# Optimization experiments

Measured on AMD Instinct MI355X. Metric: run time of the kernel, lower is better.

Reference implementation:

```python
import jax, jax.numpy as jnp
import numpy as np

B, C, H, W = 4, 512, 64, 64
CQ = C // 8


def setup_inputs() -> dict:
    key = jax.random.key(0)
    k1, k2, k3, k4, k5 = jax.random.split(key, 5)
    return {
        "x": jax.random.normal(k1, (B, C, H, W), dtype=jnp.float32),
        "Wq": jax.random.normal(k2, (CQ, C), dtype=jnp.float32) * (2.0 / C) ** 0.5,
        "Wk": jax.random.normal(k3, (CQ, C), dtype=jnp.float32) * (2.0 / C) ** 0.5,
        "Wv": jax.random.normal(k4, (C, C), dtype=jnp.float32) * (2.0 / C) ** 0.5,
        "gamma": jax.random.normal(k5, (1,), dtype=jnp.float32),
    }


def reference(x, Wq, Wk, Wv, gamma):
    b, c, h, w = x.shape
    n = h * w
    xf = x.reshape(b, c, n)                       # (B, C, N)
    # 1x1 convs (bias=False, norm=identity) == channel matmuls
    q = jnp.einsum('qc,bcn->bnq', Wq, xf)         # (B, N, Cq) -- proj_query permuted
    k = jnp.einsum('qc,bcm->bqm', Wk, xf)         # (B, Cq, N) -- proj_key
    energy = jnp.einsum('bnq,bqm->bnm', q, k)     # (B, N, N)
    attn = jax.nn.softmax(energy, axis=-1)        # softmax over keys (last dim)
    v = jnp.einsum('dc,bcm->bdm', Wv, xf)         # (B, C, N) -- proj_value
    # out = bmm(V, attn^T): out[b,d,n] = sum_m V[b,d,m] * attn[b,n,m]
    out = jnp.einsum('bdm,bnm->bdn', v, attn).reshape(b, c, h, w)
    return gamma * out + x
```

## Files before the change

kernel.cpp:

```cpp
#include <hip/hip_runtime.h>

#define B_  4
#define C_  512
#define CQ_ 64
#define N_  4096
#define LOG2E 1.44269504088896f

typedef _Float16 half8 __attribute__((ext_vector_type(8)));
typedef _Float16 half4 __attribute__((ext_vector_type(4)));
typedef float    f32x4 __attribute__((ext_vector_type(4)));

__device__ __forceinline__ void g2l16(const void* g, void* l) {
  __builtin_amdgcn_global_load_lds(
      (const __attribute__((address_space(1))) void*)g,
      (__attribute__((address_space(3))) void*)l, 16, 0, 0);
}

__global__ __launch_bounds__(256) void wcvt_kernel(
    const float* __restrict__ Wq, const float* __restrict__ Wk,
    const float* __restrict__ Wv, _Float16* __restrict__ Wh)
{
  const int row = blockIdx.x;
  const float* src;
  float s = 1.0f;
  if (row < 64)       { src = Wq + (size_t)row * C_; s = LOG2E; }
  else if (row < 128) { src = Wk + (size_t)(row - 64) * C_; }
  else                { src = Wv + (size_t)(row - 128) * C_; }
  for (int c = threadIdx.x; c < C_; c += 256)
    Wh[(size_t)row * C_ + c] = (_Float16)(src[c] * s);
}

__global__ __launch_bounds__(256) void proj_kernel(
    const float* __restrict__ x, const _Float16* __restrict__ Wh,
    _Float16* __restrict__ Qh, _Float16* __restrict__ Kh, _Float16* __restrict__ Vh)
{
  __shared__ _Float16 xs[32][520];
  __shared__ _Float16 vs[64][40];

  const int tid = threadIdx.x;
  const int wid = tid >> 6, lane = tid & 63, ln = lane & 15, lh = lane >> 4;

  const int wg = (blockIdx.x & 7) * 64 + (blockIdx.x >> 3);
  const int b  = wg >> 7;
  const int n0 = (wg & 127) * 32;

  {
    const int nn = (tid & 7) * 4;
    const int c0 = tid >> 3;
    #pragma unroll 4
    for (int cc = 0; cc < 16; ++cc) {
      const int c = cc * 32 + c0;
      f32x4 v = *(const f32x4*)&x[((size_t)b * C_ + c) * N_ + n0 + nn];
      #pragma unroll
      for (int u = 0; u < 4; ++u) xs[nn + u][c] = (_Float16)v[u];
    }
  }
  __syncthreads();

  for (int chT = 0; chT < 10; ++chT) {
    f32x4 acc[2] = {};
    const _Float16* wrow = Wh + (size_t)(chT * 64 + wid * 16 + ln) * C_;

    #pragma unroll 4
    for (int kt = 0; kt < C_; kt += 32) {
      half8 a = *(const half8*)&wrow[kt + lh * 8];
      #pragma unroll
      for (int ct = 0; ct < 2; ++ct) {
        half8 bf = *(const half8*)&xs[ct * 16 + ln][kt + lh * 8];
        acc[ct] = __builtin_amdgcn_mfma_f32_16x16x32_f16(a, bf, acc[ct], 0, 0, 0);
      }
    }

    if (chT < 2) {
      #pragma unroll
      for (int ct = 0; ct < 2; ++ct) {
        const int n = n0 + ct * 16 + ln;
        #pragma unroll
        for (int j = 0; j < 4; ++j) {
          const int chL = wid * 16 + lh * 4 + j;
          const _Float16 v = (_Float16)acc[ct][j];
          if (chT == 0) Qh[((size_t)b * N_ + n) * CQ_ + chL] = v;
          else          Kh[((size_t)b * N_ + n) * CQ_ + chL] = v;
        }
      }
    } else {
      __syncthreads();
      #pragma unroll
      for (int ct = 0; ct < 2; ++ct)
        #pragma unroll
        for (int j = 0; j < 4; ++j)
          vs[wid * 16 + lh * 4 + j][ct * 16 + ln] = (_Float16)acc[ct][j];
      __syncthreads();
      const int row = tid >> 2, cb = (tid & 3) * 8;
      *(half8*)&Vh[((size_t)b * C_ + (chT - 2) * 64 + row) * N_ + n0 + cb] =
          *(const half8*)&vs[row][cb];
    }
  }
}

__global__ __launch_bounds__(512, 2) void stats_kernel(
    const _Float16* __restrict__ Qh, const _Float16* __restrict__ Kh,
    float* __restrict__ m_g, float* __restrict__ il_g)
{
  __shared__ float Ms[8][64];
  __shared__ float Ss[8][64];

  const int tid = threadIdx.x;
  const int wid = tid >> 6, lane = tid & 63, ln = lane & 15, lh = lane >> 4;
  const int b  = blockIdx.x >> 6;
  const int qb = (blockIdx.x & 63) * 64;

  half8 qf[4][2];
  #pragma unroll
  for (int rt = 0; rt < 4; ++rt)
    #pragma unroll
    for (int h = 0; h < 2; ++h)
      qf[rt][h] = *(const half8*)&Qh[((size_t)b * N_ + qb + rt * 16 + ln) * CQ_ + h * 32 + lh * 8];

  float mx[4] = {-3.0e38f, -3.0e38f, -3.0e38f, -3.0e38f};
  float sm[4] = {0.f, 0.f, 0.f, 0.f};

  const _Float16* kp = Kh + ((size_t)b * N_ + wid * 16 + ln) * CQ_ + lh * 8;

  half8 k0 = *(const half8*)kp;
  half8 k1 = *(const half8*)(kp + 32);

  for (int it = 0; it < 32; ++it) {
    half8 kn0, kn1;
    if (it < 31) {
      const _Float16* kq = kp + (size_t)((it + 1) * 128) * CQ_;
      kn0 = *(const half8*)kq;
      kn1 = *(const half8*)(kq + 32);
    }
    #pragma unroll
    for (int rt = 0; rt < 4; ++rt) {
      f32x4 e = {};
      e = __builtin_amdgcn_mfma_f32_16x16x32_f16(k0, qf[rt][0], e, 0, 0, 0);
      e = __builtin_amdgcn_mfma_f32_16x16x32_f16(k1, qf[rt][1], e, 0, 0, 0);
      const float m1 = fmaxf(fmaxf(e[0], e[1]), fmaxf(e[2], e[3]));
      const float mn = fmaxf(mx[rt], m1);
      sm[rt] = sm[rt] * exp2f(mx[rt] - mn)
             + exp2f(e[0] - mn) + exp2f(e[1] - mn)
             + exp2f(e[2] - mn) + exp2f(e[3] - mn);
      mx[rt] = mn;
    }
    k0 = kn0; k1 = kn1;
  }

  #pragma unroll
  for (int rt = 0; rt < 4; ++rt) {
    float m = mx[rt], s = sm[rt];
    #pragma unroll
    for (int mask = 16; mask <= 32; mask <<= 1) {
      const float om = __shfl_xor(m, mask);
      const float os = __shfl_xor(s, mask);
      const float mn = fmaxf(m, om);
      s = s * exp2f(m - mn) + os * exp2f(om - mn);
      m = mn;
    }
    if (lane < 16) { Ms[wid][rt * 16 + lane] = m; Ss[wid][rt * 16 + lane] = s; }
  }
  __syncthreads();
  if (tid < 64) {
    float m = Ms[0][tid], s = Ss[0][tid];
    #pragma unroll
    for (int w = 1; w < 8; ++w) {
      const float om = Ms[w][tid], os = Ss[w][tid];
      const float mn = fmaxf(m, om);
      s = s * exp2f(m - mn) + os * exp2f(om - mn);
      m = mn;
    }
    m_g[(size_t)b * N_ + qb + tid]  = m;
    il_g[(size_t)b * N_ + qb + tid] = 1.0f / s;
  }
}

__global__ __launch_bounds__(256) void pwrite_kernel(
    const _Float16* __restrict__ Qh, const _Float16* __restrict__ Kh,
    const float* __restrict__ m_g, const float* __restrict__ il_g,
    _Float16* __restrict__ P, int b0)
{
  __shared__ _Float16 Pl[64 * 260];

  const int tid = threadIdx.x;
  const int wid = tid >> 6, lane = tid & 63, ln = lane & 15, lh = lane >> 4;
  const int mb = blockIdx.x * 256;
  const int qb = blockIdx.y * 64;
  const int bz = blockIdx.z;
  const int b  = b0 + bz;

  float m_l[4], il_l[4];
  #pragma unroll
  for (int rt = 0; rt < 4; ++rt) {
    m_l[rt]  = m_g [(size_t)b * N_ + qb + rt * 16 + ln];
    il_l[rt] = il_g[(size_t)b * N_ + qb + rt * 16 + ln];
  }

  half8 qf[4][2];
  #pragma unroll
  for (int rt = 0; rt < 4; ++rt)
    #pragma unroll
    for (int h = 0; h < 2; ++h)
      qf[rt][h] = *(const half8*)&Qh[((size_t)b * N_ + qb + rt * 16 + ln) * CQ_ + h * 32 + lh * 8];

  half8 kf[4][2];
  #pragma unroll
  for (int ms = 0; ms < 4; ++ms)
    #pragma unroll
    for (int h = 0; h < 2; ++h)
      kf[ms][h] = *(const half8*)&Kh[((size_t)b * N_ + mb + wid * 64 + ms * 16 + ln) * CQ_ + h * 32 + lh * 8];

  #pragma unroll
  for (int ms = 0; ms < 4; ++ms) {
    #pragma unroll
    for (int rt = 0; rt < 4; ++rt) {
      f32x4 e = {};
      e = __builtin_amdgcn_mfma_f32_16x16x32_f16(kf[ms][0], qf[rt][0], e, 0, 0, 0);
      e = __builtin_amdgcn_mfma_f32_16x16x32_f16(kf[ms][1], qf[rt][1], e, 0, 0, 0);
      half4 pv;
      #pragma unroll
      for (int j = 0; j < 4; ++j)
        pv[j] = (_Float16)(exp2f(e[j] - m_l[rt]) * il_l[rt]);
      *(half4*)&Pl[(rt * 16 + ln) * 260 + wid * 64 + ms * 16 + lh * 4] = pv;
    }
  }
  __syncthreads();

  const int row = tid >> 2;
  const int cb  = (tid & 3) * 8;
  #pragma unroll
  for (int i = 0; i < 8; ++i) {
    half8 v = *(const half8*)&Pl[row * 260 + cb + i * 32];
    *(half8*)&P[((size_t)bz * N_ + qb + row) * N_ + mb + cb + i * 32] = v;
  }
}

__global__ __launch_bounds__(512) void pv_kernel(
    const float* __restrict__ x, const _Float16* __restrict__ Vh,
    const _Float16* __restrict__ P, const float* __restrict__ gamma,
    float* __restrict__ out, int b0, int nwg)
{
  __shared__ _Float16 As[3][256 * 64];
  __shared__ _Float16 Bs[3][128 * 64];

  const int tid = threadIdx.x;
  const int wid = tid >> 6, lane = tid & 63, ln = lane & 15, lh = lane >> 4;

  const int q8 = nwg >> 3;
  const int wg = (blockIdx.x & 7) * q8 + (blockIdx.x >> 3);
  const int dt = wg & 1;
  const int nt = (wg >> 1) & 31;
  const int bz = wg >> 6;
  const int b  = b0 + bz;
  const int d0 = dt * 256, n0 = nt * 128;

  const _Float16* Ab = Vh + ((size_t)b * C_ + d0) * N_;
  const _Float16* Bb = P  + ((size_t)bz * N_ + n0) * N_;

  const int srow   = lane >> 3;
  const int schunk = lane & 7;
  const _Float16* aSrc[4];
  const _Float16* bSrc[2];
  #pragma unroll
  for (int r = 0; r < 4; ++r) {
    const int row = r * 64 + wid * 8 + srow;
    aSrc[r] = Ab + (size_t)row * N_ + ((schunk ^ (row & 7)) << 3);
  }
  #pragma unroll
  for (int r = 0; r < 2; ++r) {
    const int row = r * 64 + wid * 8 + srow;
    bSrc[r] = Bb + (size_t)row * N_ + ((schunk ^ (row & 7)) << 3);
  }

  auto stage = [&](int buf, int t) {
    const int m0 = t << 6;
    #pragma unroll
    for (int r = 0; r < 4; ++r)
      g2l16(aSrc[r] + m0, (char*)&As[buf][0] + r * 8192 + wid * 1024);
    #pragma unroll
    for (int r = 0; r < 2; ++r)
      g2l16(bSrc[r] + m0, (char*)&Bs[buf][0] + r * 8192 + wid * 1024);
  };

  const int wr = wid >> 1, wc = wid & 1;
  f32x4 acc[4][4] = {};
  const int swl = ln & 7;

  stage(0, 0);
  stage(1, 1);

  for (int t = 0; t < 64; ++t) {
    if (t < 63) { asm volatile("s_waitcnt vmcnt(6)" ::: "memory"); }
    else        { asm volatile("s_waitcnt vmcnt(0)" ::: "memory"); }
    __builtin_amdgcn_s_barrier();
    __builtin_amdgcn_sched_barrier(0);

    const int buf = t % 3;
    const _Float16* Ar = &As[buf][0];
    const _Float16* Br = &Bs[buf][0];

    half8 a[4][2], bq[4][2];
    #pragma unroll
    for (int ft = 0; ft < 4; ++ft) {
      const int row = wr * 64 + ft * 16 + ln;
      #pragma unroll
      for (int kk = 0; kk < 2; ++kk)
        a[ft][kk] = *(const half8*)&Ar[row * 64 + ((((kk << 2) | lh) ^ swl) << 3)];
    }
    #pragma unroll
    for (int gt = 0; gt < 4; ++gt) {
      const int row = wc * 64 + gt * 16 + ln;
      #pragma unroll
      for (int kk = 0; kk < 2; ++kk)
        bq[gt][kk] = *(const half8*)&Br[row * 64 + ((((kk << 2) | lh) ^ swl) << 3)];
    }

    if (t < 62) stage((t + 2) % 3, t + 2);

    #pragma unroll
    for (int kk = 0; kk < 2; ++kk)
      #pragma unroll
      for (int ft = 0; ft < 4; ++ft)
        #pragma unroll
        for (int gt = 0; gt < 4; ++gt)
          acc[ft][gt] = __builtin_amdgcn_mfma_f32_16x16x32_f16(a[ft][kk], bq[gt][kk], acc[ft][gt], 0, 0, 0);
  }

  const float g = gamma[0];
  #pragma unroll
  for (int ft = 0; ft < 4; ++ft) {
    #pragma unroll
    for (int gt = 0; gt < 4; ++gt) {
      #pragma unroll
      for (int j = 0; j < 4; ++j) {
        const int d = d0 + wr * 64 + ft * 16 + lh * 4 + j;
        const int n = n0 + wc * 64 + gt * 16 + ln;
        const size_t idx = ((size_t)b * C_ + d) * N_ + n;
        out[idx] = g * acc[ft][gt][j] + x[idx];
      }
    }
  }
}

extern "C" void kernel_launch(void* const* d_in, const int* in_sizes, int n_in,
                              void* d_out, int out_size, void* d_ws, size_t ws_size,
                              hipStream_t stream) {
  const float* x     = (const float*)d_in[0];
  const float* Wq    = (const float*)d_in[1];
  const float* Wk    = (const float*)d_in[2];
  const float* Wv    = (const float*)d_in[3];
  const float* gamma = (const float*)d_in[4];
  float* out = (float*)d_out;

  _Float16* Qh = (_Float16*)d_ws;
  _Float16* Kh = Qh + (size_t)B_ * N_ * CQ_;
  _Float16* Vh = Kh + (size_t)B_ * N_ * CQ_;
  float* m_g   = (float*)(Vh + (size_t)B_ * C_ * N_);
  float* il_g  = m_g + (size_t)B_ * N_;
  _Float16* Wh = (_Float16*)(il_g + (size_t)B_ * N_);
  _Float16* P  = Wh + (size_t)640 * C_;

  const size_t fixed = (size_t)((char*)P - (char*)d_ws);
  const int nb = (ws_size >= fixed + (size_t)B_ * N_ * N_ * sizeof(_Float16)) ? 4 : 2;

  wcvt_kernel<<<dim3(640), 256, 0, stream>>>(Wq, Wk, Wv, Wh);
  proj_kernel<<<dim3(512), 256, 0, stream>>>(x, Wh, Qh, Kh, Vh);
  stats_kernel<<<dim3(256), 512, 0, stream>>>(Qh, Kh, m_g, il_g);

  for (int b0 = 0; b0 < B_; b0 += nb) {
    pwrite_kernel<<<dim3(16, 64, nb), 256, 0, stream>>>(Qh, Kh, m_g, il_g, P, b0);
    pv_kernel<<<dim3(nb * 64), 512, 0, stream>>>(x, Vh, P, gamma, out, b0, nb * 64);
  }
}
```

Baseline: 185.6 us.

## Fuse probability computation into PV kernel, eliminating materialized attention matrix

Replaces the separate pwrite and pv kernels with one fused kernel. Each workgroup recomputes QK^T scores per key tile from staged K, applies the precomputed max and inverse sum to form P in LDS, and then multiplies by V. This removes the write and reread of the full fp16 N×N attention matrix in global memory. In exchange, each workgroup recomputes scores (the two d-tiles duplicate that work), adds an extra barrier per iteration, and serialises exp work with the MFMA pipeline.

```diff
diff --git a/kernel.cpp b/kernel.cpp
--- a/kernel.cpp
+++ b/kernel.cpp
@@ -175,166 +175,138 @@
   }
 }
 
-__global__ __launch_bounds__(256) void pwrite_kernel(
-    const _Float16* __restrict__ Qh, const _Float16* __restrict__ Kh,
+__global__ __launch_bounds__(512) void fpv_kernel(
+    const float* __restrict__ x, const _Float16* __restrict__ Qh,
+    const _Float16* __restrict__ Kh, const _Float16* __restrict__ Vh,
     const float* __restrict__ m_g, const float* __restrict__ il_g,
-    _Float16* __restrict__ P, int b0)
+    const float* __restrict__ gamma, float* __restrict__ out)
 {
-  __shared__ _Float16 Pl[64 * 260];
+  __shared__ _Float16 As[3][256 * 64];
+  __shared__ _Float16 Ks[3][64 * 64];
+  __shared__ _Float16 Ps[128 * 64];
 
   const int tid = threadIdx.x;
   const int wid = tid >> 6, lane = tid & 63, ln = lane & 15, lh = lane >> 4;
-  const int mb = blockIdx.x * 256;
-  const int qb = blockIdx.y * 64;
-  const int bz = blockIdx.z;
-  const int b  = b0 + bz;
-
-  float m_l[4], il_l[4];
-  #pragma unroll
-  for (int rt = 0; rt < 4; ++rt) {
-    m_l[rt]  = m_g [(size_t)b * N_ + qb + rt * 16 + ln];
-    il_l[rt] = il_g[(size_t)b * N_ + qb + rt * 16 + ln];
-  }
-
-  half8 qf[4][2];
-  #pragma unroll
-  for (int rt = 0; rt < 4; ++rt)
-    #pragma unroll
-    for (int h = 0; h < 2; ++h)
-      qf[rt][h] = *(const half8*)&Qh[((size_t)b * N_ + qb + rt * 16 + ln) * CQ_ + h * 32 + lh * 8];
-
-  half8 kf[4][2];
-  #pragma unroll
-  for (int ms = 0; ms < 4; ++ms)
-    #pragma unroll
-    for (int h = 0; h < 2; ++h)
-      kf[ms][h] = *(const half8*)&Kh[((size_t)b * N_ + mb + wid * 64 + ms * 16 + ln) * CQ_ + h * 32 + lh * 8];
-
-  #pragma unroll
-  for (int ms = 0; ms < 4; ++ms) {
-    #pragma unroll
-    for (int rt = 0; rt < 4; ++rt) {
-      f32x4 e = {};
-      e = __builtin_amdgcn_mfma_f32_16x16x32_f16(kf[ms][0], qf[rt][0], e, 0, 0, 0);
-      e = __builtin_amdgcn_mfma_f32_16x16x32_f16(kf[ms][1], qf[rt][1], e, 0, 0, 0);
-      half4 pv;
-      #pragma unroll
-      for (int j = 0; j < 4; ++j)
-        pv[j] = (_Float16)(exp2f(e[j] - m_l[rt]) * il_l[rt]);
-      *(half4*)&Pl[(rt * 16 + ln) * 260 + wid * 64 + ms * 16 + lh * 4] = pv;
-    }
-  }
-  __syncthreads();
-
-  const int row = tid >> 2;
-  const int cb  = (tid & 3) * 8;
-  #pragma unroll
-  for (int i = 0; i < 8; ++i) {
-    half8 v = *(const half8*)&Pl[row * 260 + cb + i * 32];
-    *(half8*)&P[((size_t)bz * N_ + qb + row) * N_ + mb + cb + i * 32] = v;
-  }
-}
-
-__global__ __launch_bounds__(512) void pv_kernel(
-    const float* __restrict__ x, const _Float16* __restrict__ Vh,
-    const _Float16* __restrict__ P, const float* __restrict__ gamma,
-    float* __restrict__ out, int b0, int nwg)
-{
-  __shared__ _Float16 As[3][256 * 64];
-  __shared__ _Float16 Bs[3][128 * 64];
-
-  const int tid = threadIdx.x;
-  const int wid = tid >> 6, lane = tid & 63, ln = lane & 15, lh = lane >> 4;
-
-  const int q8 = nwg >> 3;
-  const int wg = (blockIdx.x & 7) * q8 + (blockIdx.x >> 3);
+
+  const int wg = (blockIdx.x & 7) * 32 + (blockIdx.x >> 3);
   const int dt = wg & 1;
   const int nt = (wg >> 1) & 31;
-  const int bz = wg >> 6;
-  const int b  = b0 + bz;
+  const int b  = wg >> 6;
   const int d0 = dt * 256, n0 = nt * 128;
 
-  const _Float16* Ab = Vh + ((size_t)b * C_ + d0) * N_;
-  const _Float16* Bb = P  + ((size_t)bz * N_ + n0) * N_;
+  const float m2  = m_g [(size_t)b * N_ + n0 + wid * 16 + ln];
+  const float il2 = il_g[(size_t)b * N_ + n0 + wid * 16 + ln];
+
+  half8 qf[2];
+  #pragma unroll
+  for (int h = 0; h < 2; ++h)
+    qf[h] = *(const half8*)&Qh[((size_t)b * N_ + n0 + wid * 16 + ln) * CQ_ + h * 32 + lh * 8];
 
   const int srow   = lane >> 3;
   const int schunk = lane & 7;
   const _Float16* aSrc[4];
-  const _Float16* bSrc[2];
   #pragma unroll
   for (int r = 0; r < 4; ++r) {
     const int row = r * 64 + wid * 8 + srow;
-    aSrc[r] = Ab + (size_t)row * N_ + ((schunk ^ (row & 7)) << 3);
-  }
-  #pragma unroll
-  for (int r = 0; r < 2; ++r) {
-    const int row = r * 64 + wid * 8 + srow;
-    bSrc[r] = Bb + (size_t)row * N_ + ((schunk ^ (row & 7)) << 3);
+    aSrc[r] = Vh + ((size_t)b * C_ + d0 + row) * N_ + ((schunk ^ (row & 7)) << 3);
+  }
+  const _Float16* kSrc;
+  {
+    const int row = wid * 8 + srow;
+    kSrc = Kh + ((size_t)b * N_ + row) * CQ_ + ((schunk ^ (row & 7)) << 3);
   }
 
   auto stage = [&](int buf, int t) {
-    const int m0 = t << 6;
+    const int mA = t << 6;
     #pragma unroll
     for (int r = 0; r < 4; ++r)
-      g2l16(aSrc[r] + m0, (char*)&As[buf][0] + r * 8192 + wid * 1024);
-    #pragma unroll
-    for (int r = 0; r < 2; ++r)
-      g2l16(bSrc[r] + m0, (char*)&Bs[buf][0] + r * 8192 + wid * 1024);
+      g2l16(aSrc[r] + mA, (char*)&As[buf][0] + r * 8192 + wid * 1024);
+    g2l16(kSrc + (size_t)(t << 6) * CQ_, (char*)&Ks[buf][0] + wid * 1024);
   };
 
-  const int wr = wid >> 1, wc = wid & 1;
+  const int dr = wid >> 1, nc = wid & 1;
+  const int swl = ln & 7;
   f32x4 acc[4][4] = {};
-  const int swl = ln & 7;
 
   stage(0, 0);
   stage(1, 1);
 
   for (int t = 0; t < 64; ++t) {
-    if (t < 63) { asm volatile("s_waitcnt vmcnt(6)" ::: "memory"); }
+    if (t < 63) { asm volatile("s_waitcnt vmcnt(5)" ::: "memory"); }
     else        { asm volatile("s_waitcnt vmcnt(0)" ::: "memory"); }
     __builtin_amdgcn_s_barrier();
     __builtin_amdgcn_sched_barrier(0);
 
     const int buf = t % 3;
-    const _Float16* Ar = &As[buf][0];
-    const _Float16* Br = &Bs[buf][0];
-
-    half8 a[4][2], bq[4][2];
-    #pragma unroll
-    for (int ft = 0; ft < 4; ++ft) {
-      const int row = wr * 64 + ft * 16 + ln;
-      #pragma unroll
-      for (int kk = 0; kk < 2; ++kk)
-        a[ft][kk] = *(const half8*)&Ar[row * 64 + ((((kk << 2) | lh) ^ swl) << 3)];
-    }
+
+    {
+      const _Float16* Kr = &Ks[buf][0];
+      half8 kf[4][2];
+      #pragma unroll
+      for (int kt = 0; kt < 4; ++kt) {
+        const int key = kt * 16 + ln;
+        #pragma unroll
+        for (int c = 0; c < 2; ++c)
+          kf[kt][c] = *(const half8*)&Kr[key * 64 + ((((c << 2) | lh) ^ swl) << 3)];
+      }
+
+      if (t < 62) stage((t + 2) % 3, t + 2);
+
+      #pragma unroll
+      for (int kt = 0; kt < 4; ++kt) {
+        f32x4 e = {};
+        e = __builtin_amdgcn_mfma_f32_16x16x32_f16(kf[kt][0], qf[0], e, 0, 0, 0);
+        e = __builtin_amdgcn_mfma_f32_16x16x32_f16(kf[kt][1], qf[1], e, 0, 0, 0);
+        half4 pv;
+        #pragma unroll
+        for (int j = 0; j < 4; ++j)
+          pv[j] = (_Float16)(exp2f(e[j] - m2) * il2);
+        *(half4*)((char*)&Ps[(wid * 16 + ln) * 64]
+                  + ((((kt << 1) | (lh >> 1)) ^ swl) << 4) + ((lh & 1) << 3)) = pv;
+      }
+    }
+
+    asm volatile("s_waitcnt lgkmcnt(0)" ::: "memory");
+    __builtin_amdgcn_sched_barrier(0);
+    __builtin_amdgcn_s_barrier();
+    __builtin_amdgcn_sched_barrier(0);
+
+    {
+      const _Float16* Ar = &As[buf][0];
+      half8 a[4][2], bq[4][2];
+      #pragma unroll
+      for (int ft = 0; ft < 4; ++ft) {
+        const int row = dr * 64 + ft * 16 + ln;
+        #pragma unroll
+        for (int c = 0; c < 2; ++c)
+          a[ft][c] = *(const half8*)&Ar[row * 64 + ((((c << 2) | lh) ^ swl) << 3)];
+      }
+      #pragma unroll
+      for (int gt = 0; gt < 4; ++gt) {
+        const int q = nc * 64 + gt * 16 + ln;
+        #pragma unroll
+        for (int c = 0; c < 2; ++c)
+          bq[gt][c] = *(const half8*)&Ps[q * 64 + ((((c << 2) | lh) ^ swl) << 3)];
+      }
+      #pragma unroll
+      for (int c = 0; c < 2; ++c)
+        #pragma unroll
+        for (int ft = 0; ft < 4; ++ft)
+          #pragma unroll
+          for (int gt = 0; gt < 4; ++gt)
+            acc[ft][gt] = __builtin_amdgcn_mfma_f32_16x16x32_f16(a[ft][c], bq[gt][c], acc[ft][gt], 0, 0, 0);
+    }
+  }
+
+  const float g = gamma[0];
+  #pragma unroll
+  for (int ft = 0; ft < 4; ++ft) {
     #pragma unroll
     for (int gt = 0; gt < 4; ++gt) {
-      const int row = wc * 64 + gt * 16 + ln;
-      #pragma unroll
-      for (int kk = 0; kk < 2; ++kk)
-        bq[gt][kk] = *(const half8*)&Br[row * 64 + ((((kk << 2) | lh) ^ swl) << 3)];
-    }
-
-    if (t < 62) stage((t + 2) % 3, t + 2);
-
-    #pragma unroll
-    for (int kk = 0; kk < 2; ++kk)
-      #pragma unroll
-      for (int ft = 0; ft < 4; ++ft)
-        #pragma unroll
-        for (int gt = 0; gt < 4; ++gt)
-          acc[ft][gt] = __builtin_amdgcn_mfma_f32_16x16x32_f16(a[ft][kk], bq[gt][kk], acc[ft][gt], 0, 0, 0);
-  }
-
-  const float g = gamma[0];
-  #pragma unroll
-  for (int ft = 0; ft < 4; ++ft) {
-    #pragma unroll
-    for (int gt = 0; gt < 4; ++gt) {
       #pragma unroll
       for (int j = 0; j < 4; ++j) {
-        const int d = d0 + wr * 64 + ft * 16 + lh * 4 + j;
-        const int n = n0 + wc * 64 + gt * 16 + ln;
+        const int d = d0 + dr * 64 + ft * 16 + lh * 4 + j;
+        const int n = n0 + nc * 64 + gt * 16 + ln;
         const size_t idx = ((size_t)b * C_ + d) * N_ + n;
         out[idx] = g * acc[ft][gt][j] + x[idx];
       }
@@ -358,17 +330,9 @@
   float* m_g   = (float*)(Vh + (size_t)B_ * C_ * N_);
   float* il_g  = m_g + (size_t)B_ * N_;
   _Float16* Wh = (_Float16*)(il_g + (size_t)B_ * N_);
-  _Float16* P  = Wh + (size_t)640 * C_;
-
-  const size_t fixed = (size_t)((char*)P - (char*)d_ws);
-  const int nb = (ws_size >= fixed + (size_t)B_ * N_ * N_ * sizeof(_Float16)) ? 4 : 2;
 
   wcvt_kernel<<<dim3(640), 256, 0, stream>>>(Wq, Wk, Wv, Wh);
   proj_kernel<<<dim3(512), 256, 0, stream>>>(x, Wh, Qh, Kh, Vh);
   stats_kernel<<<dim3(256), 512, 0, stream>>>(Qh, Kh, m_g, il_g);
-
-  for (int b0 = 0; b0 < B_; b0 += nb) {
-    pwrite_kernel<<<dim3(16, 64, nb), 256, 0, stream>>>(Qh, Kh, m_g, il_g, P, b0);
-    pv_kernel<<<dim3(nb * 64), 512, 0, stream>>>(x, Vh, P, gamma, out, b0, nb * 64);
-  }
-}
+  fpv_kernel<<<dim3(256), 512, 0, stream>>>(x, Qh, Kh, Vh, m_g, il_g, gamma, out);
+}
```

Result: slower. 195.2 us (+5.2%).

## Split PV GEMM K-step into two half phases with interleaved staging and setprio

Applied to the files above, without the earlier changes.

Splits each 64-wide K tile of the output GEMM into two 32-wide halves. Each half reads its own LDS fragments, issues half of the next-next tile's global-to-LDS loads, and runs its MFMAs under raised wave priority, with an extra barrier between the halves. The aim is to interleave load issue with MFMA work, lower register pressure from fragment buffers, and let waves in the MFMA phase keep priority. The risk is the extra barrier per iteration. The vmcnt(6) wait still matches six outstanding loads per stage, now issued in two groups of three.

```diff
diff --git a/kernel.cpp b/kernel.cpp
--- a/kernel.cpp
+++ b/kernel.cpp
@@ -272,22 +272,25 @@
     bSrc[r] = Bb + (size_t)row * N_ + ((schunk ^ (row & 7)) << 3);
   }
 
-  auto stage = [&](int buf, int t) {
+  auto stageA = [&](int buf, int t) {
     const int m0 = t << 6;
-    #pragma unroll
-    for (int r = 0; r < 4; ++r)
-      g2l16(aSrc[r] + m0, (char*)&As[buf][0] + r * 8192 + wid * 1024);
-    #pragma unroll
-    for (int r = 0; r < 2; ++r)
-      g2l16(bSrc[r] + m0, (char*)&Bs[buf][0] + r * 8192 + wid * 1024);
+    g2l16(aSrc[0] + m0, (char*)&As[buf][0] + 0 * 8192 + wid * 1024);
+    g2l16(aSrc[1] + m0, (char*)&As[buf][0] + 1 * 8192 + wid * 1024);
+    g2l16(bSrc[0] + m0, (char*)&Bs[buf][0] + 0 * 8192 + wid * 1024);
+  };
+  auto stageB = [&](int buf, int t) {
+    const int m0 = t << 6;
+    g2l16(aSrc[2] + m0, (char*)&As[buf][0] + 2 * 8192 + wid * 1024);
+    g2l16(aSrc[3] + m0, (char*)&As[buf][0] + 3 * 8192 + wid * 1024);
+    g2l16(bSrc[1] + m0, (char*)&Bs[buf][0] + 1 * 8192 + wid * 1024);
   };
 
   const int wr = wid >> 1, wc = wid & 1;
   f32x4 acc[4][4] = {};
   const int swl = ln & 7;
 
-  stage(0, 0);
-  stage(1, 1);
+  stageA(0, 0); stageB(0, 0);
+  stageA(1, 1); stageB(1, 1);
 
   for (int t = 0; t < 64; ++t) {
     if (t < 63) { asm volatile("s_waitcnt vmcnt(6)" ::: "memory"); }
@@ -299,31 +302,53 @@
     const _Float16* Ar = &As[buf][0];
     const _Float16* Br = &Bs[buf][0];
 
-    half8 a[4][2], bq[4][2];
-    #pragma unroll
-    for (int ft = 0; ft < 4; ++ft) {
-      const int row = wr * 64 + ft * 16 + ln;
-      #pragma unroll
-      for (int kk = 0; kk < 2; ++kk)
-        a[ft][kk] = *(const half8*)&Ar[row * 64 + ((((kk << 2) | lh) ^ swl) << 3)];
-    }
-    #pragma unroll
-    for (int gt = 0; gt < 4; ++gt) {
-      const int row = wc * 64 + gt * 16 + ln;
-      #pragma unroll
-      for (int kk = 0; kk < 2; ++kk)
-        bq[gt][kk] = *(const half8*)&Br[row * 64 + ((((kk << 2) | lh) ^ swl) << 3)];
-    }
-
-    if (t < 62) stage((t + 2) % 3, t + 2);
-
-    #pragma unroll
-    for (int kk = 0; kk < 2; ++kk)
+    {
+      half8 a[4], bq[4];
+      #pragma unroll
+      for (int ft = 0; ft < 4; ++ft) {
+        const int row = wr * 64 + ft * 16 + ln;
+        a[ft] = *(const half8*)&Ar[row * 64 + ((lh ^ swl) << 3)];
+      }
+      #pragma unroll
+      for (int gt = 0; gt < 4; ++gt) {
+        const int row = wc * 64 + gt * 16 + ln;
+        bq[gt] = *(const half8*)&Br[row * 64 + ((lh ^ swl) << 3)];
+      }
+      if (t < 62) stageA((t + 2) % 3, t + 2);
+
+      __builtin_amdgcn_s_setprio(1);
       #pragma unroll
       for (int ft = 0; ft < 4; ++ft)
         #pragma unroll
         for (int gt = 0; gt < 4; ++gt)
-          acc[ft][gt] = __builtin_amdgcn_mfma_f32_16x16x32_f16(a[ft][kk], bq[gt][kk], acc[ft][gt], 0, 0, 0);
+          acc[ft][gt] = __builtin_amdgcn_mfma_f32_16x16x32_f16(a[ft], bq[gt], acc[ft][gt], 0, 0, 0);
+      __builtin_amdgcn_s_setprio(0);
+    }
+    __builtin_amdgcn_s_barrier();
+    __builtin_amdgcn_sched_barrier(0);
+
+    {
+      half8 a[4], bq[4];
+      #pragma unroll
+      for (int ft = 0; ft < 4; ++ft) {
+        const int row = wr * 64 + ft * 16 + ln;
+        a[ft] = *(const half8*)&Ar[row * 64 + (((4 | lh) ^ swl) << 3)];
+      }
+      #pragma unroll
+      for (int gt = 0; gt < 4; ++gt) {
+        const int row = wc * 64 + gt * 16 + ln;
+        bq[gt] = *(const half8*)&Br[row * 64 + (((4 | lh) ^ swl) << 3)];
+      }
+      if (t < 62) stageB((t + 2) % 3, t + 2);
+
+      __builtin_amdgcn_s_setprio(1);
+      #pragma unroll
+      for (int ft = 0; ft < 4; ++ft)
+        #pragma unroll
+        for (int gt = 0; gt < 4; ++gt)
+          acc[ft][gt] = __builtin_amdgcn_mfma_f32_16x16x32_f16(a[ft], bq[gt], acc[ft][gt], 0, 0, 0);
+      __builtin_amdgcn_s_setprio(0);
+    }
   }
 
   const float g = gamma[0];
```

Measured after the change: 187.6 us. About the same (+1.1%).
